# Optimization experiments

Measured on AMD Instinct MI355X. Metric: run time of the kernel, lower is better.

## Reference

```python
import jax, jax.numpy as jnp
import numpy as np

N_ORDER = 256
PRED_LEN = 192
SEQ_LEN = 768
ENC_IN = 21
BATCH = 16
MULTISCALE = [1, 2, 4]
MODES = 32  # min(32, min(pred_len, seq_len)//2)


def _transition(N):
    Q = np.arange(N, dtype=np.float64)
    R = (2 * Q + 1)[:, None]
    j, i = np.meshgrid(Q, Q)
    A = np.where(i < j, -1, (-1.0) ** (i - j + 1)) * R
    B = (-1.0) ** Q[:, None] * R
    return A, B


def _bilinear(A, B, dt):
    # scipy cont2discrete(method='bilinear'): Ad=(I-dt/2 A)^-1 (I+dt/2 A), Bd=(I-dt/2 A)^-1 dt B
    N = A.shape[0]
    I = np.eye(N)
    ima = I - (dt / 2.0) * A
    Ad = np.linalg.solve(ima, I + (dt / 2.0) * A)
    Bd = np.linalg.solve(ima, dt * B)
    return Ad, Bd.squeeze(-1)


def _legendre_eval(N, x):
    # Legendre P_n(x) via three-term recurrence; returns [len(x), N]
    T = x.shape[0]
    P = np.zeros((N, T))
    P[0] = 1.0
    if N > 1:
        P[1] = x
    for n in range(2, N):
        P[n] = ((2 * n - 1) * x * P[n - 1] - (n - 1) * P[n - 2]) / n
    return P.T


def setup_inputs() -> dict:
    key = jax.random.key(0)
    ks = jax.random.split(key, 12)
    inp = {"x_enc": jax.random.normal(ks[0], (BATCH, SEQ_LEN, ENC_IN), dtype=jnp.float32)}
    Ac, Bc = _transition(N_ORDER)
    scale = 1.0 / (N_ORDER * N_ORDER)
    for idx, m in enumerate(MULTISCALE):
        dt = 1.0 / PRED_LEN / m
        Ad, Bd = _bilinear(Ac, Bc, dt)
        vals = np.arange(0.0, 1.0, dt)
        E = _legendre_eval(N_ORDER, 1.0 - 2.0 * vals)
        inp[f"A{idx}"] = jnp.asarray(Ad, jnp.float32)
        inp[f"B{idx}"] = jnp.asarray(Bd, jnp.float32)
        inp[f"E{idx}"] = jnp.asarray(E, jnp.float32)
        inp[f"Wr{idx}"] = scale * jax.random.uniform(ks[1 + 2 * idx], (N_ORDER, N_ORDER, MODES), dtype=jnp.float32)
        inp[f"Wi{idx}"] = scale * jax.random.uniform(ks[2 + 2 * idx], (N_ORDER, N_ORDER, MODES), dtype=jnp.float32)
    inp["mlp_w"] = 0.1 * jax.random.normal(ks[10], (1, len(MULTISCALE)), dtype=jnp.float32)
    inp["mlp_b"] = jnp.zeros((1,), jnp.float32)
    return inp


def _hippo(x, A, Bv):
    # x: [B, E, L]; c_t = c_{t-1} @ A^T + f_t * B  (F.linear(c, A) == c @ A.T)
    def step(c, f):
        c = c @ A.T + f[..., None] * Bv
        return c, c
    c0 = jnp.zeros(x.shape[:-1] + (A.shape[0],), x.dtype)
    _, cs = jax.lax.scan(step, c0, jnp.moveaxis(x, -1, 0))
    return jnp.moveaxis(cs, 0, -1)  # [B, E, N, L]


def _spec_conv(x, Wr, Wi):
    # x: [B, E, N_in, L]; keep first MODES rfft modes, complex channel mix, irfft
    L = x.shape[-1]
    a = jnp.fft.rfft(x, axis=-1)[..., :MODES]
    W = (Wr + 1j * Wi).astype(jnp.complex64)
    out = jnp.einsum('bjix,iox->bjox', a, W)
    nf = L // 2 + 1
    out_full = jnp.pad(out, ((0, 0), (0, 0), (0, 0), (0, nf - MODES)))
    return jnp.fft.irfft(out_full, n=L, axis=-1)


def reference(x_enc, A0, B0, E0, Wr0, Wi0, A1, B1, E1, Wr1, Wi1, A2, B2, E2, Wr2, Wi2, mlp_w, mlp_b):
    params = [(A0, B0, E0, Wr0, Wi0), (A1, B1, E1, Wr1, Wi1), (A2, B2, E2, Wr2, Wi2)]
    x_decs = []
    for m, (A, Bv, E, Wr, Wi) in zip(MULTISCALE, params):
        x_in = x_enc[:, -m * PRED_LEN:]                      # [B, L, E]
        c = _hippo(jnp.transpose(x_in, (0, 2, 1)), A, Bv)    # [B, E, N, L]
        out1 = _spec_conv(c, Wr, Wi)                         # [B, E, N, L]
        x_dec_c = out1[:, :, :, PRED_LEN - 1]                # seq_len >= pred_len, jump_dist=0
        x_decs.append(x_dec_c @ E[-PRED_LEN:].T)             # [B, E, pred_len]
    x_dec = jnp.stack(x_decs, axis=-1)                       # [B, E, pred_len, 3]
    out = x_dec @ mlp_w[0] + mlp_b[0]                        # Linear(3,1) then squeeze
    return jnp.transpose(out, (0, 2, 1))                     # [B, pred_len, E]
```

## Files before the change

### kernel.cpp

```cpp
#include <hip/hip_runtime.h>
#include <math.h>

#define PI_F 3.14159265358979323846f

#define W_OFF    0
#define AP_OFF   344064
#define KT_OFF   737280
#define KTOT_OFF 995328
#define Y_OFF    1142784
#define S_OFF    1142784
#define F_OFF    1732608
#define QT_OFF   10579968
#define WS_FLOATS 27095040

__device__ __forceinline__ int off_w_f(int s)  { return 49152  * ((1 << s) - 1); }
__device__ __forceinline__ int qoff_f(int s)   { return 2359296 * ((1 << s) - 1); }
__device__ __forceinline__ int ktoff_f(int s)  { return 36864  * ((1 << s) - 1); }
__device__ __forceinline__ int foff_f(int s)   { return 1179648 * ((1 << s) - 1); }

template<bool BT>
__device__ __forceinline__ void gemm_tile(const float* __restrict__ A,
                                          const float* __restrict__ B,
                                          float* __restrict__ C,
                                          int M, int N, int ldc, int m0, int n0)
{
    __shared__ float As[16][68];
    __shared__ float Bs[16][68];
    const int tid = threadIdx.x;
    const int tx = tid & 15;
    const int ty = tid >> 4;
    const int r  = tid >> 2;
    const int kq = (tid & 3) << 2;

    float acc[4][4] = {{0.f,0.f,0.f,0.f},{0.f,0.f,0.f,0.f},
                       {0.f,0.f,0.f,0.f},{0.f,0.f,0.f,0.f}};

    for (int kk = 0; kk < 256; kk += 16) {
        float4 av = make_float4(0.f, 0.f, 0.f, 0.f);
        if (m0 + r < M)
            av = *(const float4*)(A + (size_t)(m0 + r) * 256 + kk + kq);
        As[kq + 0][r] = av.x; As[kq + 1][r] = av.y;
        As[kq + 2][r] = av.z; As[kq + 3][r] = av.w;

        if (BT) {
            float4 bv = make_float4(0.f, 0.f, 0.f, 0.f);
            if (n0 + r < N)
                bv = *(const float4*)(B + (size_t)(n0 + r) * 256 + kk + kq);
            Bs[kq + 0][r] = bv.x; Bs[kq + 1][r] = bv.y;
            Bs[kq + 2][r] = bv.z; Bs[kq + 3][r] = bv.w;
        } else {
            const int kb = tid >> 4;
            const int j4 = (tid & 15) << 2;
            float4 bv = *(const float4*)(B + (size_t)(kk + kb) * 256 + n0 + j4);
            *(float4*)(&Bs[kb][j4]) = bv;
        }
        __syncthreads();

        #pragma unroll
        for (int k = 0; k < 16; ++k) {
            float4 a4 = *(const float4*)(&As[k][ty << 2]);
            float4 b4 = *(const float4*)(&Bs[k][tx << 2]);
            acc[0][0] = fmaf(a4.x, b4.x, acc[0][0]);
            acc[0][1] = fmaf(a4.x, b4.y, acc[0][1]);
            acc[0][2] = fmaf(a4.x, b4.z, acc[0][2]);
            acc[0][3] = fmaf(a4.x, b4.w, acc[0][3]);
            acc[1][0] = fmaf(a4.y, b4.x, acc[1][0]);
            acc[1][1] = fmaf(a4.y, b4.y, acc[1][1]);
            acc[1][2] = fmaf(a4.y, b4.z, acc[1][2]);
            acc[1][3] = fmaf(a4.y, b4.w, acc[1][3]);
            acc[2][0] = fmaf(a4.z, b4.x, acc[2][0]);
            acc[2][1] = fmaf(a4.z, b4.y, acc[2][1]);
            acc[2][2] = fmaf(a4.z, b4.z, acc[2][2]);
            acc[2][3] = fmaf(a4.z, b4.w, acc[2][3]);
            acc[3][0] = fmaf(a4.w, b4.x, acc[3][0]);
            acc[3][1] = fmaf(a4.w, b4.y, acc[3][1]);
            acc[3][2] = fmaf(a4.w, b4.z, acc[3][2]);
            acc[3][3] = fmaf(a4.w, b4.w, acc[3][3]);
        }
        __syncthreads();
    }

    #pragma unroll
    for (int u = 0; u < 4; ++u) {
        int row = m0 + (ty << 2) + u;
        if (row < M) {
            float4 cv = make_float4(acc[u][0], acc[u][1], acc[u][2], acc[u][3]);
            *(float4*)(C + (size_t)row * ldc + n0 + (tx << 2)) = cv;
        }
    }
}

__device__ __forceinline__ void gemm64x128(const float* __restrict__ A,
                                           const float* __restrict__ B,
                                           float* __restrict__ C, int ldc)
{
    __shared__ float As[16][68];
    __shared__ float Bs[16][132];

    const int tid = threadIdx.x;
    const int tx  = tid & 15;
    const int ty  = tid >> 4;
    const int ra  = tid >> 1;
    const int kq8 = (tid & 1) << 3;

    float acc[2][2][4][4];
    #pragma unroll
    for (int h = 0; h < 2; ++h)
        #pragma unroll
        for (int g = 0; g < 2; ++g)
            #pragma unroll
            for (int u = 0; u < 4; ++u)
                #pragma unroll
                for (int v = 0; v < 4; ++v) acc[h][g][u][v] = 0.f;

    for (int kk = 0; kk < 256; kk += 16) {
        const float* ap = A + (size_t)ra * 256 + kk + kq8;
        float4 a0 = *(const float4*)(ap);
        float4 a1 = *(const float4*)(ap + 4);
        As[kq8 + 0][ra] = a0.x; As[kq8 + 1][ra] = a0.y;
        As[kq8 + 2][ra] = a0.z; As[kq8 + 3][ra] = a0.w;
        As[kq8 + 4][ra] = a1.x; As[kq8 + 5][ra] = a1.y;
        As[kq8 + 6][ra] = a1.z; As[kq8 + 7][ra] = a1.w;

        const float* bp = B + (size_t)tid * 256 + kk;
        float4 b0 = *(const float4*)(bp);
        float4 b1 = *(const float4*)(bp + 4);
        float4 b2 = *(const float4*)(bp + 8);
        float4 b3 = *(const float4*)(bp + 12);
        Bs[ 0][tid] = b0.x; Bs[ 1][tid] = b0.y; Bs[ 2][tid] = b0.z; Bs[ 3][tid] = b0.w;
        Bs[ 4][tid] = b1.x; Bs[ 5][tid] = b1.y; Bs[ 6][tid] = b1.z; Bs[ 7][tid] = b1.w;
        Bs[ 8][tid] = b2.x; Bs[ 9][tid] = b2.y; Bs[10][tid] = b2.z; Bs[11][tid] = b2.w;
        Bs[12][tid] = b3.x; Bs[13][tid] = b3.y; Bs[14][tid] = b3.z; Bs[15][tid] = b3.w;
        __syncthreads();

        #pragma unroll
        for (int kq = 0; kq < 16; ++kq) {
            float4 aA = *(const float4*)(&As[kq][4 * ty]);
            float4 aB = *(const float4*)(&As[kq][4 * ty + 32]);
            float4 bA = *(const float4*)(&Bs[kq][4 * tx]);
            float4 bB = *(const float4*)(&Bs[kq][4 * tx + 64]);
            float af[8] = {aA.x, aA.y, aA.z, aA.w, aB.x, aB.y, aB.z, aB.w};
            float bf[8] = {bA.x, bA.y, bA.z, bA.w, bB.x, bB.y, bB.z, bB.w};
            #pragma unroll
            for (int h = 0; h < 2; ++h)
                #pragma unroll
                for (int u = 0; u < 4; ++u)
                    #pragma unroll
                    for (int g = 0; g < 2; ++g)
                        #pragma unroll
                        for (int v = 0; v < 4; ++v)
                            acc[h][g][u][v] = fmaf(af[h * 4 + u], bf[g * 4 + v],
                                                   acc[h][g][u][v]);
        }
        __syncthreads();
    }

    #pragma unroll
    for (int h = 0; h < 2; ++h)
        #pragma unroll
        for (int u = 0; u < 4; ++u) {
            int row = 4 * ty + 32 * h + u;
            #pragma unroll
            for (int g = 0; g < 2; ++g) {
                float4 cv = make_float4(acc[h][g][u][0], acc[h][g][u][1],
                                        acc[h][g][u][2], acc[h][g][u][3]);
                *(float4*)(C + (size_t)row * ldc + 4 * tx + 64 * g) = cv;
            }
        }
}

__global__ void k_init(const float* B0, const float* B1, const float* B2, float* ws)
{
    int s = blockIdx.x;
    const float* Bv = (s == 0) ? B0 : (s == 1) ? B1 : B2;
    ws[W_OFF + off_w_f(s) + threadIdx.x] = Bv[threadIdx.x];
}

__global__ void k_level(int n, const float* A0, const float* A1, const float* A2,
                        float* ws)
{
    int s = blockIdx.z;
    int L = 192 << s;
    const float* Ain = (s == 0) ? A0 : (s == 1) ? A1 : A2;
    float* wbase = ws + W_OFF + off_w_f(s);
    float* bufA  = ws + AP_OFF + s * 131072;
    float* bufB  = bufA + 65536;
    const float* src = (n == 0) ? Ain : (((n - 1) & 1) ? bufB : bufA);

    int y = blockIdx.y;
    if (y < 4) {
        int p2 = 1 << n;
        if (p2 >= L) return;
        int cnt = min(p2, L - p2);
        int m0 = y * 64;
        if (m0 >= cnt) return;
        gemm_tile<true>(wbase, src, wbase + (size_t)p2 * 256,
                        cnt, 256, 256, m0, blockIdx.x * 64);
    } else {
        if ((2 << n) >= L) return;
        float* dst = (n & 1) ? bufB : bufA;
        gemm_tile<false>(src, src, dst, 256, 256, 256, (y - 4) * 64, blockIdx.x * 64);
    }
}

__global__ void k_transpose(const float* Wr0, const float* Wi0,
                            const float* Wr1, const float* Wi1,
                            const float* Wr2, const float* Wi2, float* ws)
{
    __shared__ float t[256][33];
    int bid = blockIdx.x;
    int i  = bid & 255;
    int ri = (bid >> 8) & 1;
    int s  = bid >> 9;
    const float* W;
    if (s == 0)      W = ri ? Wi0 : Wr0;
    else if (s == 1) W = ri ? Wi1 : Wr1;
    else             W = ri ? Wi2 : Wr2;

    const int tid = threadIdx.x;
    const float* slab = W + (size_t)i * 8192;
    #pragma unroll
    for (int j = 0; j < 8; ++j) {
        int f = j * 1024 + tid * 4;
        float4 v = *(const float4*)(slab + f);
        int o = f >> 5;
        int k = f & 31;
        t[o][k + 0] = v.x; t[o][k + 1] = v.y;
        t[o][k + 2] = v.z; t[o][k + 3] = v.w;
    }
    __syncthreads();

    int sri = s * 2 + ri;
    #pragma unroll
    for (int k = 0; k < 32; ++k) {
        ws[QT_OFF + (size_t)(sri * 32 + k) * 65536 + (size_t)i * 256 + tid] = t[tid][k];
    }
}

__global__ void __launch_bounds__(128, 4)
k_gemm_Y4(const float* E0, const float* E1, const float* E2, float* __restrict__ ws)
{
    const int s  = blockIdx.z;
    const int L  = 192 << s;
    const int zz = blockIdx.x >> 1;
    const int n0 = (blockIdx.x & 1) * 128;
    const int z  = s * 64 + zz;
    const int m0 = blockIdx.y * 64;
    const float* E = (s == 0) ? E0 : (s == 1) ? E1 : E2;

    const float* Ap = E + (size_t)(L - 192) * 256 + (size_t)m0 * 256;
    const float* Bp = ws + QT_OFF + (size_t)z * 65536 + (size_t)n0 * 256;
    float* Cp = ws + Y_OFF + (size_t)z * 49152 + (size_t)m0 * 256 + n0;
    gemm64x128(Ap, Bp, Cp, 256);
}

__global__ void __launch_bounds__(128, 4)
k_gemm_Q4(float* __restrict__ ws)
{
    const int y = blockIdx.y;
    int s, yt;
    if (y < 3)      { s = 0; yt = y; }
    else if (y < 9) { s = 1; yt = y - 3; }
    else            { s = 2; yt = y - 9; }
    const int m0 = yt * 64;
    const int n0 = blockIdx.x * 128;

    const float* Ap = ws + W_OFF + off_w_f(s) + (size_t)m0 * 256;
    const float* Bp = ws + Y_OFF + (size_t)s * 3145728 + (size_t)n0 * 256;
    float* Cp = ws + QT_OFF + qoff_f(s) + (size_t)m0 * 12288 + n0;
    gemm64x128(Ap, Bp, Cp, 12288);
}

__global__ void k_scanA(float* __restrict__ ws)
{
    const int c = blockIdx.x;
    const int k = blockIdx.y;
    const int s = blockIdx.z;
    const int L = 192 << s;
    const int C = L >> 4;
    const int p = threadIdx.x;

    __shared__ float twc[768], tws[768];
    for (int m = p; m < L; m += 192) {
        float ang = -2.f * PI_F * (float)m / (float)L;
        float ss, cc; sincosf(ang, &ss, &cc);
        twc[m] = cc; tws[m] = ss;
    }
    __syncthreads();

    const float* Qr = ws + QT_OFF + qoff_f(s) + (size_t)k * 192;
    const float* Qi = Qr + 6144;

    float ar = 0.f, ai = 0.f;
    const int d0 = c * C;
    int ph = (k * d0) % L;
    for (int j = 0; j < C; ++j) {
        int d = d0 + j;
        float qr = Qr[(size_t)d * 12288 + p];
        float qi = Qi[(size_t)d * 12288 + p];
        float cc = twc[ph], sn = tws[ph];
        ar = fmaf(cc, qr, fmaf(-sn, qi, ar));
        ai = fmaf(cc, qi, fmaf( sn, qr, ai));
        ph += k; if (ph >= L) ph -= L;
    }
    size_t sb = (size_t)((s * 32 + k) * 16 + c) * 384;
    ws[S_OFF + sb + p]       = ar;
    ws[S_OFF + sb + 192 + p] = ai;
}

__global__ void k_scanB(float* __restrict__ ws)
{
    const int c = blockIdx.x;
    const int k = blockIdx.y;
    const int s = blockIdx.z;
    const int L = 192 << s;
    const int C = L >> 4;
    const int p = threadIdx.x;

    __shared__ float twc[768], tws[768];
    for (int m = p; m < L; m += 192) {
        float ang = -2.f * PI_F * (float)m / (float)L;
        float ss, cc; sincosf(ang, &ss, &cc);
        twc[m] = cc; tws[m] = ss;
    }
    __syncthreads();

    float ar = 0.f, ai = 0.f;
    size_t sbase = (size_t)(s * 32 + k) * 16 * 384;
    for (int c2 = 0; c2 < c; ++c2) {
        ar += ws[S_OFF + sbase + (size_t)c2 * 384 + p];
        ai += ws[S_OFF + sbase + (size_t)c2 * 384 + 192 + p];
    }

    const float ck = ((k == 0) ? 1.f : 2.f) / (float)L;
    const float* Qr = ws + QT_OFF + qoff_f(s) + (size_t)k * 192;
    const float* Qi = Qr + 6144;
    float* F = ws + F_OFF + foff_f(s);

    const int d0 = c * C;
    int ph = (k * d0) % L;
    int m1 = d0 + 192 - L; if (m1 < 0) m1 += L;
    int ph2 = (k * m1) % L;
    for (int j = 0; j < C; ++j) {
        int d = d0 + j;
        float qr = Qr[(size_t)d * 12288 + p];
        float qi = Qi[(size_t)d * 12288 + p];
        float cc = twc[ph], sn = tws[ph];
        ar = fmaf(cc, qr, fmaf(-sn, qi, ar));
        ai = fmaf(cc, qi, fmaf( sn, qr, ai));
        float f = ck * fmaf(twc[ph2], ar, tws[ph2] * ai);
        int sidx = L - 1 - d;
        F[((size_t)sidx * 32 + k) * 192 + p] = f;
        ph  += k; if (ph  >= L) ph  -= L;
        ph2 += k; if (ph2 >= L) ph2 -= L;
    }
}

__global__ void k_kred(float* __restrict__ ws)
{
    int bid = blockIdx.x;
    int s, sidx;
    if (bid < 192)      { s = 0; sidx = bid; }
    else if (bid < 576) { s = 1; sidx = bid - 192; }
    else                { s = 2; sidx = bid - 576; }
    int p = threadIdx.x;
    const float* F = ws + F_OFF + foff_f(s) + (size_t)sidx * 32 * 192;
    float sum = 0.f;
    #pragma unroll
    for (int k = 0; k < 32; ++k)
        sum += F[k * 192 + p];
    ws[KT_OFF + ktoff_f(s) + (size_t)sidx * 192 + p] = sum;
}

__global__ void k_combine(float* ws, const float* mw)
{
    int idx = blockIdx.x * 256 + threadIdx.x;
    if (idx >= 147456) return;
    int tau = idx / 192;
    int p   = idx - tau * 192;
    float sum = 0.f;
    #pragma unroll
    for (int s = 0; s < 3; ++s) {
        int L = 192 << s;
        int off = 768 - L;
        if (tau >= off)
            sum = fmaf(mw[s], ws[KT_OFF + ktoff_f(s) + (size_t)(tau - off) * 192 + p], sum);
    }
    ws[KTOT_OFF + idx] = sum;
}

__global__ void k_out(const float* __restrict__ x, const float* __restrict__ ws,
                      const float* __restrict__ mb, float* __restrict__ out)
{
    int bid = blockIdx.x;
    int b = bid / 21;
    int c = bid - b * 21;
    __shared__ float xl[768];
    for (int t = threadIdx.x; t < 768; t += 192)
        xl[t] = x[((size_t)b * 768 + t) * 21 + c];
    __syncthreads();

    int p = threadIdx.x;
    const float* K = ws + KTOT_OFF;
    float acc = 0.f;
    for (int tau = 0; tau < 768; ++tau)
        acc = fmaf(xl[tau], K[(size_t)tau * 192 + p], acc);
    out[((size_t)b * 192 + p) * 21 + c] = acc + mb[0];
}

extern "C" void kernel_launch(void* const* d_in, const int* in_sizes, int n_in,
                              void* d_out, int out_size, void* d_ws, size_t ws_size,
                              hipStream_t stream)
{
    const float* x   = (const float*)d_in[0];
    const float* A0  = (const float*)d_in[1];
    const float* B0  = (const float*)d_in[2];
    const float* E0  = (const float*)d_in[3];
    const float* Wr0 = (const float*)d_in[4];
    const float* Wi0 = (const float*)d_in[5];
    const float* A1  = (const float*)d_in[6];
    const float* B1  = (const float*)d_in[7];
    const float* E1  = (const float*)d_in[8];
    const float* Wr1 = (const float*)d_in[9];
    const float* Wi1 = (const float*)d_in[10];
    const float* A2  = (const float*)d_in[11];
    const float* B2  = (const float*)d_in[12];
    const float* E2  = (const float*)d_in[13];
    const float* Wr2 = (const float*)d_in[14];
    const float* Wi2 = (const float*)d_in[15];
    const float* mw  = (const float*)d_in[16];
    const float* mb  = (const float*)d_in[17];
    float* ws  = (float*)d_ws;
    float* out = (float*)d_out;

    if (ws_size < (size_t)WS_FLOATS * sizeof(float)) {
        hipMemsetAsync(d_out, 0, (size_t)out_size * sizeof(float), stream);
        return;
    }

    k_init<<<3, 256, 0, stream>>>(B0, B1, B2, ws);
    for (int n = 0; n < 10; ++n)
        k_level<<<dim3(4, 8, 3), 256, 0, stream>>>(n, A0, A1, A2, ws);
    k_transpose<<<1536, 256, 0, stream>>>(Wr0, Wi0, Wr1, Wi1, Wr2, Wi2, ws);
    k_gemm_Y4<<<dim3(128, 3, 3), 128, 0, stream>>>(E0, E1, E2, ws);
    k_gemm_Q4<<<dim3(96, 21), 128, 0, stream>>>(ws);
    k_scanA<<<dim3(16, 32, 3), 192, 0, stream>>>(ws);
    k_scanB<<<dim3(16, 32, 3), 192, 0, stream>>>(ws);
    k_kred<<<1344, 192, 0, stream>>>(ws);
    k_combine<<<576, 256, 0, stream>>>(ws, mw);
    k_out<<<336, 192, 0, stream>>>(x, ws, mb, out);
}
```

Measured before the change: 429.0 us.

## Fuse scan pass B with k-reduction and re-chunk scans into fixed 12-step blocks

The second scan pass now loops over all 32 modes inside one block and accumulates the per-mode outputs in registers. This removes the large intermediate F buffer and the separate k_kred reduction kernel. Scan chunks are fixed at 12 steps with more chunks per scale, and the Q GEMM uses a 256-thread variant with fewer accumulators per thread. The trade-off is that the fused scanB has far fewer blocks (64x3) doing 32x serial work, with prefix sums over up to 64 chunks per mode, which may hurt parallelism.

```diff
diff --git a/kernel.cpp b/kernel.cpp
--- a/kernel.cpp
+++ b/kernel.cpp
@@ -9,14 +9,12 @@
 #define KTOT_OFF 995328
 #define Y_OFF    1142784
 #define S_OFF    1142784
-#define F_OFF    1732608
 #define QT_OFF   10579968
 #define WS_FLOATS 27095040
 
 __device__ __forceinline__ int off_w_f(int s)  { return 49152  * ((1 << s) - 1); }
 __device__ __forceinline__ int qoff_f(int s)   { return 2359296 * ((1 << s) - 1); }
 __device__ __forceinline__ int ktoff_f(int s)  { return 36864  * ((1 << s) - 1); }
-__device__ __forceinline__ int foff_f(int s)   { return 1179648 * ((1 << s) - 1); }
 
 template<bool BT>
 __device__ __forceinline__ void gemm_tile(const float* __restrict__ A,
@@ -90,9 +88,76 @@
     }
 }
 
-__device__ __forceinline__ void gemm64x128(const float* __restrict__ A,
-                                           const float* __restrict__ B,
-                                           float* __restrict__ C, int ldc)
+__device__ __forceinline__ void gemm64x128_q(const float* __restrict__ A,
+                                             const float* __restrict__ B,
+                                             float* __restrict__ C, int ldc)
+{
+    __shared__ float As[16][68];
+    __shared__ float Bs[16][132];
+
+    const int tid = threadIdx.x;
+    const int tx = tid & 15;
+    const int ty = tid >> 4;
+    const int ra  = tid >> 2;
+    const int kqa = (tid & 3) << 2;
+    const int rb  = tid >> 1;
+    const int kq8 = (tid & 1) << 3;
+
+    float acc[2][4][4];
+    #pragma unroll
+    for (int g = 0; g < 2; ++g)
+        #pragma unroll
+        for (int u = 0; u < 4; ++u)
+            #pragma unroll
+            for (int v = 0; v < 4; ++v) acc[g][u][v] = 0.f;
+
+    for (int kk = 0; kk < 256; kk += 16) {
+        float4 av = *(const float4*)(A + (size_t)ra * 256 + kk + kqa);
+        As[kqa + 0][ra] = av.x; As[kqa + 1][ra] = av.y;
+        As[kqa + 2][ra] = av.z; As[kqa + 3][ra] = av.w;
+
+        const float* bp = B + (size_t)rb * 256 + kk + kq8;
+        float4 b0 = *(const float4*)(bp);
+        float4 b1 = *(const float4*)(bp + 4);
+        Bs[kq8 + 0][rb] = b0.x; Bs[kq8 + 1][rb] = b0.y;
+        Bs[kq8 + 2][rb] = b0.z; Bs[kq8 + 3][rb] = b0.w;
+        Bs[kq8 + 4][rb] = b1.x; Bs[kq8 + 5][rb] = b1.y;
+        Bs[kq8 + 6][rb] = b1.z; Bs[kq8 + 7][rb] = b1.w;
+        __syncthreads();
+
+        #pragma unroll
+        for (int kq = 0; kq < 16; ++kq) {
+            float4 a   = *(const float4*)(&As[kq][4 * ty]);
+            float4 b0v = *(const float4*)(&Bs[kq][4 * tx]);
+            float4 b1v = *(const float4*)(&Bs[kq][4 * tx + 64]);
+            float af[4] = {a.x, a.y, a.z, a.w};
+            float bf[8] = {b0v.x, b0v.y, b0v.z, b0v.w, b1v.x, b1v.y, b1v.z, b1v.w};
+            #pragma unroll
+            for (int g = 0; g < 2; ++g)
+                #pragma unroll
+                for (int u = 0; u < 4; ++u)
+                    #pragma unroll
+                    for (int v = 0; v < 4; ++v)
+                        acc[g][u][v] = fmaf(af[u], bf[g * 4 + v], acc[g][u][v]);
+        }
+        __syncthreads();
+    }
+
+    #pragma unroll
+    for (int u = 0; u < 4; ++u) {
+        int row = 4 * ty + u;
+        #pragma unroll
+        for (int g = 0; g < 2; ++g) {
+            float4 cv = make_float4(acc[g][u][0], acc[g][u][1],
+                                    acc[g][u][2], acc[g][u][3]);
+            *(float4*)(C + (size_t)row * ldc + 4 * tx + 64 * g) = cv;
+        }
+    }
+}
+
+__device__ __forceinline__ void gemm64x128_y(const float* __restrict__ A,
+                                             const float* __restrict__ B,
+                                             float* __restrict__ C, int ldc)
 {
     __shared__ float As[16][68];
     __shared__ float Bs[16][132];
@@ -251,10 +316,10 @@
     const float* Ap = E + (size_t)(L - 192) * 256 + (size_t)m0 * 256;
     const float* Bp = ws + QT_OFF + (size_t)z * 65536 + (size_t)n0 * 256;
     float* Cp = ws + Y_OFF + (size_t)z * 49152 + (size_t)m0 * 256 + n0;
-    gemm64x128(Ap, Bp, Cp, 256);
-}
-
-__global__ void __launch_bounds__(128, 4)
+    gemm64x128_y(Ap, Bp, Cp, 256);
+}
+
+__global__ void __launch_bounds__(256, 4)
 k_gemm_Q4(float* __restrict__ ws)
 {
     const int y = blockIdx.y;
@@ -268,7 +333,7 @@
     const float* Ap = ws + W_OFF + off_w_f(s) + (size_t)m0 * 256;
     const float* Bp = ws + Y_OFF + (size_t)s * 3145728 + (size_t)n0 * 256;
     float* Cp = ws + QT_OFF + qoff_f(s) + (size_t)m0 * 12288 + n0;
-    gemm64x128(Ap, Bp, Cp, 12288);
+    gemm64x128_q(Ap, Bp, Cp, 12288);
 }
 
 __global__ void k_scanA(float* __restrict__ ws)
@@ -276,8 +341,9 @@
     const int c = blockIdx.x;
     const int k = blockIdx.y;
     const int s = blockIdx.z;
+    const int NC = 16 << s;
+    if (c >= NC) return;
     const int L = 192 << s;
-    const int C = L >> 4;
     const int p = threadIdx.x;
 
     __shared__ float twc[768], tws[768];
@@ -292,9 +358,10 @@
     const float* Qi = Qr + 6144;
 
     float ar = 0.f, ai = 0.f;
-    const int d0 = c * C;
+    const int d0 = c * 12;
     int ph = (k * d0) % L;
-    for (int j = 0; j < C; ++j) {
+    #pragma unroll
+    for (int j = 0; j < 12; ++j) {
         int d = d0 + j;
         float qr = Qr[(size_t)d * 12288 + p];
         float qi = Qi[(size_t)d * 12288 + p];
@@ -303,18 +370,18 @@
         ai = fmaf(cc, qi, fmaf( sn, qr, ai));
         ph += k; if (ph >= L) ph -= L;
     }
-    size_t sb = (size_t)((s * 32 + k) * 16 + c) * 384;
+    size_t sb = (size_t)((s * 32 + k) * 64 + c) * 384;
     ws[S_OFF + sb + p]       = ar;
     ws[S_OFF + sb + 192 + p] = ai;
 }
 
-__global__ void k_scanB(float* __restrict__ ws)
+__global__ void k_scanBR(float* __restrict__ ws)
 {
     const int c = blockIdx.x;
-    const int k = blockIdx.y;
-    const int s = blockIdx.z;
+    const int s = blockIdx.y;
+    const int NC = 16 << s;
+    if (c >= NC) return;
     const int L = 192 << s;
-    const int C = L >> 4;
     const int p = threadIdx.x;
 
     __shared__ float twc[768], tws[768];
@@ -325,51 +392,48 @@
     }
     __syncthreads();
 
-    float ar = 0.f, ai = 0.f;
-    size_t sbase = (size_t)(s * 32 + k) * 16 * 384;
-    for (int c2 = 0; c2 < c; ++c2) {
-        ar += ws[S_OFF + sbase + (size_t)c2 * 384 + p];
-        ai += ws[S_OFF + sbase + (size_t)c2 * 384 + 192 + p];
-    }
-
-    const float ck = ((k == 0) ? 1.f : 2.f) / (float)L;
-    const float* Qr = ws + QT_OFF + qoff_f(s) + (size_t)k * 192;
-    const float* Qi = Qr + 6144;
-    float* F = ws + F_OFF + foff_f(s);
-
-    const int d0 = c * C;
-    int ph = (k * d0) % L;
+    float fa[12];
+    #pragma unroll
+    for (int j = 0; j < 12; ++j) fa[j] = 0.f;
+
+    const int d0 = c * 12;
     int m1 = d0 + 192 - L; if (m1 < 0) m1 += L;
-    int ph2 = (k * m1) % L;
-    for (int j = 0; j < C; ++j) {
-        int d = d0 + j;
-        float qr = Qr[(size_t)d * 12288 + p];
-        float qi = Qi[(size_t)d * 12288 + p];
-        float cc = twc[ph], sn = tws[ph];
-        ar = fmaf(cc, qr, fmaf(-sn, qi, ar));
-        ai = fmaf(cc, qi, fmaf( sn, qr, ai));
-        float f = ck * fmaf(twc[ph2], ar, tws[ph2] * ai);
-        int sidx = L - 1 - d;
-        F[((size_t)sidx * 32 + k) * 192 + p] = f;
-        ph  += k; if (ph  >= L) ph  -= L;
-        ph2 += k; if (ph2 >= L) ph2 -= L;
-    }
-}
-
-__global__ void k_kred(float* __restrict__ ws)
-{
-    int bid = blockIdx.x;
-    int s, sidx;
-    if (bid < 192)      { s = 0; sidx = bid; }
-    else if (bid < 576) { s = 1; sidx = bid - 192; }
-    else                { s = 2; sidx = bid - 576; }
-    int p = threadIdx.x;
-    const float* F = ws + F_OFF + foff_f(s) + (size_t)sidx * 32 * 192;
-    float sum = 0.f;
-    #pragma unroll
-    for (int k = 0; k < 32; ++k)
-        sum += F[k * 192 + p];
-    ws[KT_OFF + ktoff_f(s) + (size_t)sidx * 192 + p] = sum;
+
+    for (int k = 0; k < 32; ++k) {
+        float ar = 0.f, ai = 0.f;
+        size_t sbase = (size_t)((s * 32 + k) * 64) * 384;
+        for (int c2 = 0; c2 < c; ++c2) {
+            ar += ws[S_OFF + sbase + (size_t)c2 * 384 + p];
+            ai += ws[S_OFF + sbase + (size_t)c2 * 384 + 192 + p];
+        }
+
+        const float ck = ((k == 0) ? 1.f : 2.f) / (float)L;
+        const float* Qr = ws + QT_OFF + qoff_f(s) + (size_t)k * 192;
+        const float* Qi = Qr + 6144;
+
+        int ph  = (k * d0) % L;
+        int ph2 = (k * m1) % L;
+        #pragma unroll
+        for (int j = 0; j < 12; ++j) {
+            int d = d0 + j;
+            float qr = Qr[(size_t)d * 12288 + p];
+            float qi = Qi[(size_t)d * 12288 + p];
+            float cc = twc[ph], sn = tws[ph];
+            ar = fmaf(cc, qr, fmaf(-sn, qi, ar));
+            ai = fmaf(cc, qi, fmaf( sn, qr, ai));
+            float f = ck * fmaf(twc[ph2], ar, tws[ph2] * ai);
+            fa[j] += f;
+            ph  += k; if (ph  >= L) ph  -= L;
+            ph2 += k; if (ph2 >= L) ph2 -= L;
+        }
+    }
+
+    float* Kt = ws + KT_OFF + ktoff_f(s);
+    #pragma unroll
+    for (int j = 0; j < 12; ++j) {
+        int sidx = L - 1 - (d0 + j);
+        Kt[(size_t)sidx * 192 + p] = fa[j];
+    }
 }
 
 __global__ void k_combine(float* ws, const float* mw)
@@ -443,10 +507,9 @@
         k_level<<<dim3(4, 8, 3), 256, 0, stream>>>(n, A0, A1, A2, ws);
     k_transpose<<<1536, 256, 0, stream>>>(Wr0, Wi0, Wr1, Wi1, Wr2, Wi2, ws);
     k_gemm_Y4<<<dim3(128, 3, 3), 128, 0, stream>>>(E0, E1, E2, ws);
-    k_gemm_Q4<<<dim3(96, 21), 128, 0, stream>>>(ws);
-    k_scanA<<<dim3(16, 32, 3), 192, 0, stream>>>(ws);
-    k_scanB<<<dim3(16, 32, 3), 192, 0, stream>>>(ws);
-    k_kred<<<1344, 192, 0, stream>>>(ws);
+    k_gemm_Q4<<<dim3(96, 21), 256, 0, stream>>>(ws);
+    k_scanA<<<dim3(64, 32, 3), 192, 0, stream>>>(ws);
+    k_scanBR<<<dim3(64, 3), 192, 0, stream>>>(ws);
     k_combine<<<576, 256, 0, stream>>>(ws, mw);
     k_out<<<336, 192, 0, stream>>>(x, ws, mb, out);
 }
```

Measured after the change: 744.8 us. 73.6% more time.
